# Performance work log

Hardware: AMD Instinct MI355X
Metric: run time of the kernel (lower is better)

The kernel has to match this reference:

```python
import jax, jax.numpy as jnp
import numpy as np

B, N, F = 4, 3000, 128

def setup_inputs() -> dict:
    key = jax.random.key(0)
    k1, k2, k3, k4 = jax.random.split(key, 4)
    x = jax.random.normal(k1, (B, N, F), dtype=jnp.float32)
    adj = jax.random.uniform(k2, (B, N, N), dtype=jnp.float32)
    h0 = jax.random.normal(k3, (B, N, F), dtype=jnp.float32)
    stdv = 1.0 / np.sqrt(F)
    theta = jax.random.uniform(k4, (F, F), dtype=jnp.float32, minval=-stdv, maxval=stdv)
    return {
        "x": x, "adj": adj, "h0": h0, "theta": theta,
        "lamda": jnp.float32(0.5), "alpha": jnp.float32(0.1), "l": 4,
    }

def _normalize_adj(adj):
    # add self loops, then D^{-1/2} A D^{-1/2} via elementwise row/col scaling
    # (same math as diag-embed + inverse + two bmms in the original)
    n = adj.shape[1]
    adj = adj + jnp.eye(n, dtype=adj.dtype)
    deg = jnp.sum(adj, axis=2)                      # [B, N]
    d_inv_sqrt = jax.lax.rsqrt(deg)                 # [B, N]
    return d_inv_sqrt[:, :, None] * adj * d_inv_sqrt[:, None, :]

def reference(x, adj, h0, theta, lamda, alpha, l):
    adj_n = _normalize_adj(adj)
    beta = jnp.log(lamda / l + 1.0)
    hi = jnp.einsum('bnm,bmf->bnf', adj_n, x)       # aggregation
    support = (1.0 - alpha) * hi + alpha * h0       # variant=False path
    r = support
    out = beta * jnp.einsum('bnf,fg->bng', support, theta) + (1.0 - beta) * r
    return out
```

## Files before the change

kernel.cpp:

```cpp
#include <hip/hip_runtime.h>
#include <hip/hip_bf16.h>
#include <math.h>

#define BB 4
#define NN 3000
#define FF 128
#define NKC 96
#define NIT 188

typedef __bf16 bf16x8 __attribute__((ext_vector_type(8)));
typedef float  f32x4  __attribute__((ext_vector_type(4)));

__global__ __launch_bounds__(256) void k_deg(const float* __restrict__ adj,
                                             float* __restrict__ dis) {
    int wid  = (blockIdx.x * 256 + threadIdx.x) >> 6;
    int lane = threadIdx.x & 63;
    if (wid >= BB * NN) return;
    const float4* row = (const float4*)(adj + (size_t)wid * NN);
    float s = 0.f;
    for (int c = lane; c < NN / 4; c += 64) {
        float4 v = row[c];
        s += (v.x + v.y) + (v.z + v.w);
    }
    for (int off = 32; off > 0; off >>= 1) s += __shfl_down(s, off, 64);
    if (lane == 0) dis[wid] = 1.0f / sqrtf(s + 1.0f);
}

__global__ __launch_bounds__(256) void k_xpk(const float* __restrict__ x,
                                             const float* __restrict__ dis,
                                             __bf16* __restrict__ xpk) {
    int b  = blockIdx.y, kc = blockIdx.x;
    int t  = threadIdx.x, w = t >> 6, l = t & 63;
    int m  = l & 15, q = l >> 4;
    #pragma unroll
    for (int h = 0; h < 2; ++h) {
        int nt = w + h * 4;
        int f  = nt * 16 + m;
        bf16x8 v;
        #pragma unroll
        for (int j = 0; j < 8; ++j) {
            int k = kc * 32 + q * 8 + j;
            float val = 0.f;
            if (k < NN) val = dis[b * NN + k] * x[((size_t)b * NN + k) * FF + f];
            v[j] = (__bf16)val;
        }
        *(bf16x8*)(xpk + ((size_t)(b * 8 + nt) * NKC + kc) * 512 + l * 8) = v;
    }
}

__global__ __launch_bounds__(256) void k_thpk(const float* __restrict__ theta,
                                              __bf16* __restrict__ thpk) {
    int kc = blockIdx.x;
    int t  = threadIdx.x, w = t >> 6, l = t & 63;
    int m  = l & 15, q = l >> 4;
    #pragma unroll
    for (int h = 0; h < 2; ++h) {
        int nt = w + h * 4;
        bf16x8 v;
        #pragma unroll
        for (int j = 0; j < 8; ++j) {
            int k = kc * 32 + q * 8 + j;
            v[j] = (__bf16)theta[k * FF + nt * 16 + m];
        }
        *(bf16x8*)(thpk + ((size_t)(nt * 4 + kc)) * 512 + l * 8) = v;
    }
}

__global__ __launch_bounds__(256) void k_agg(const float* __restrict__ adj,
                                             const __bf16* __restrict__ xpk,
                                             const __bf16* __restrict__ thpk,
                                             const float* __restrict__ x,
                                             const float* __restrict__ h0,
                                             const float* __restrict__ dis,
                                             float* __restrict__ out,
                                             const float* __restrict__ alpha_p,
                                             const float* __restrict__ lamda_p,
                                             const int* __restrict__ l_p) {
    __shared__ __bf16 tile[2][16][520];
    __shared__ __bf16 stile[16][136];
    const int b  = blockIdx.y;
    const int it = blockIdx.x;
    const int i0 = it * 16;
    const int t  = threadIdx.x, w = t >> 6, l = t & 63;
    const int m  = l & 15, quad = l >> 4;
    const int n0 = w * 32;
    const __bf16* B0 = xpk + ((size_t)(b * 8 + 2 * w) * NKC) * 512 + l * 8;
    const __bf16* B1 = B0 + (size_t)NKC * 512;
    f32x4 acc0 = {0.f, 0.f, 0.f, 0.f};
    f32x4 acc1 = {0.f, 0.f, 0.f, 0.f};

    float4 pu[4], pv[4];
    auto load_chunk = [&](int c) {
        int k0 = c * 512;
        #pragma unroll
        for (int i = 0; i < 4; ++i) {
            int row  = i * 4 + w;
            int irow = i0 + row;
            int col  = k0 + l * 8;
            float4 u = {0.f, 0.f, 0.f, 0.f}, v = {0.f, 0.f, 0.f, 0.f};
            if (irow < NN && col < NN) {
                const float* p = adj + ((size_t)b * NN + irow) * NN + col;
                u = *(const float4*)p;
                v = *(const float4*)(p + 4);
            }
            pu[i] = u; pv[i] = v;
        }
    };
    auto store_chunk = [&](int cb) {
        #pragma unroll
        for (int i = 0; i < 4; ++i) {
            int row = i * 4 + w;
            bf16x8 s;
            s[0] = (__bf16)pu[i].x; s[1] = (__bf16)pu[i].y;
            s[2] = (__bf16)pu[i].z; s[3] = (__bf16)pu[i].w;
            s[4] = (__bf16)pv[i].x; s[5] = (__bf16)pv[i].y;
            s[6] = (__bf16)pv[i].z; s[7] = (__bf16)pv[i].w;
            *(bf16x8*)&tile[cb][row][l * 8] = s;
        }
    };

    load_chunk(0);
    store_chunk(0);
    __syncthreads();
    for (int c = 0; c < 6; ++c) {
        int cb = c & 1;
        if (c < 5) load_chunk(c + 1);
        #pragma unroll 4
        for (int kcl = 0; kcl < 16; ++kcl) {
            int kc = c * 16 + kcl;
            bf16x8 a  = *(const bf16x8*)&tile[cb][m][kcl * 32 + quad * 8];
            bf16x8 b0 = *(const bf16x8*)(B0 + (size_t)kc * 512);
            bf16x8 b1 = *(const bf16x8*)(B1 + (size_t)kc * 512);
            acc0 = __builtin_amdgcn_mfma_f32_16x16x32_bf16(a, b0, acc0, 0, 0, 0);
            acc1 = __builtin_amdgcn_mfma_f32_16x16x32_bf16(a, b1, acc1, 0, 0, 0);
        }
        if (c < 5) store_chunk(cb ^ 1);
        __syncthreads();
    }

    const float alpha = *alpha_p;
    const float beta  = logf(*lamda_p / (float)(*l_p) + 1.0f);
    float s0v[4], s1v[4];
    #pragma unroll
    for (int r = 0; r < 4; ++r) {
        int row  = quad * 4 + r;
        int irow = i0 + row;
        float s0 = 0.f, s1 = 0.f;
        if (irow < NN) {
            float  di   = dis[b * NN + irow];
            size_t base = ((size_t)b * NN + irow) * FF;
            int c0 = n0 + m, c1 = n0 + 16 + m;
            s0 = (1.f - alpha) * (di * acc0[r] + di * di * x[base + c0]) + alpha * h0[base + c0];
            s1 = (1.f - alpha) * (di * acc1[r] + di * di * x[base + c1]) + alpha * h0[base + c1];
        }
        s0v[r] = s0; s1v[r] = s1;
        stile[row][n0 + m]      = (__bf16)s0;
        stile[row][n0 + 16 + m] = (__bf16)s1;
    }
    __syncthreads();
    f32x4 o0 = {0.f, 0.f, 0.f, 0.f};
    f32x4 o1 = {0.f, 0.f, 0.f, 0.f};
    const __bf16* T0 = thpk + (size_t)(2 * w * 4) * 512 + l * 8;
    const __bf16* T1 = T0 + 4 * 512;
    #pragma unroll
    for (int kc = 0; kc < 4; ++kc) {
        bf16x8 a   = *(const bf16x8*)&stile[m][kc * 32 + quad * 8];
        bf16x8 tb0 = *(const bf16x8*)(T0 + (size_t)kc * 512);
        bf16x8 tb1 = *(const bf16x8*)(T1 + (size_t)kc * 512);
        o0 = __builtin_amdgcn_mfma_f32_16x16x32_bf16(a, tb0, o0, 0, 0, 0);
        o1 = __builtin_amdgcn_mfma_f32_16x16x32_bf16(a, tb1, o1, 0, 0, 0);
    }
    const float omb = 1.f - beta;
    #pragma unroll
    for (int r = 0; r < 4; ++r) {
        int irow = i0 + quad * 4 + r;
        if (irow < NN) {
            size_t base = ((size_t)b * NN + irow) * FF;
            out[base + n0 + m]      = beta * o0[r] + omb * s0v[r];
            out[base + n0 + 16 + m] = beta * o1[r] + omb * s1v[r];
        }
    }
}

extern "C" void kernel_launch(void* const* d_in, const int* in_sizes, int n_in,
                              void* d_out, int out_size, void* d_ws, size_t ws_size,
                              hipStream_t stream) {
    const float* x      = (const float*)d_in[0];
    const float* adj    = (const float*)d_in[1];
    const float* h0     = (const float*)d_in[2];
    const float* theta  = (const float*)d_in[3];
    const float* lamda  = (const float*)d_in[4];
    const float* alpha  = (const float*)d_in[5];
    const int*   l      = (const int*)d_in[6];
    float* out = (float*)d_out;

    char*   ws   = (char*)d_ws;
    float*  dis  = (float*)ws;
    __bf16* xpk  = (__bf16*)(ws + 65536);
    __bf16* thpk = (__bf16*)(ws + 3276800);

    k_deg<<<dim3((BB * NN) / 4), 256, 0, stream>>>(adj, dis);
    k_thpk<<<dim3(4), 256, 0, stream>>>(theta, thpk);
    k_xpk<<<dim3(NKC, BB), 256, 0, stream>>>(x, dis, xpk);
    k_agg<<<dim3(NIT, BB), 256, 0, stream>>>(adj, xpk, thpk, x, h0, dis, out,
                                             alpha, lamda, l);
}
```

Measured before the change: 277.1 us.

## Pre-convert adjacency to padded bf16 in degree pass and async-load into LDS

The degree kernel now also writes a zero-padded bf16 copy of the adjacency matrix (rows padded to 3008, columns to 3072) while it sums each row. The aggregation kernel then reads this bf16 copy and moves it straight into shared memory with global_load_lds, dropping the register round-trip, the fp32-to-bf16 conversion and the bounds checks from its inner pipeline. The aim is to halve the bytes the main kernel reads and to overlap loads with MFMA work more cheaply. In exchange the degree pass writes an extra ~74 MB buffer, the total memory traffic stays about the same, and the code relies on a large workspace.

```diff
diff --git a/kernel.cpp b/kernel.cpp
--- a/kernel.cpp
+++ b/kernel.cpp
@@ -5,25 +5,37 @@
 #define BB 4
 #define NN 3000
 #define FF 128
+#define NP 3008
+#define CP 3072
 #define NKC 96
 #define NIT 188
 
 typedef __bf16 bf16x8 __attribute__((ext_vector_type(8)));
+typedef __bf16 bf16x4 __attribute__((ext_vector_type(4)));
 typedef float  f32x4  __attribute__((ext_vector_type(4)));
 
 __global__ __launch_bounds__(256) void k_deg(const float* __restrict__ adj,
+                                             __bf16* __restrict__ adjh,
                                              float* __restrict__ dis) {
     int wid  = (blockIdx.x * 256 + threadIdx.x) >> 6;
     int lane = threadIdx.x & 63;
-    if (wid >= BB * NN) return;
-    const float4* row = (const float4*)(adj + (size_t)wid * NN);
+    int b = wid / NP, i = wid % NP;
+    bool rowok = i < NN;
+    const float* row = adj + ((size_t)b * NN + (rowok ? i : 0)) * NN;
+    __bf16* drow = adjh + (size_t)wid * CP;
     float s = 0.f;
-    for (int c = lane; c < NN / 4; c += 64) {
-        float4 v = row[c];
+    for (int c = lane; c < CP / 4; c += 64) {
+        int col = c * 4;
+        float4 v = {0.f, 0.f, 0.f, 0.f};
+        if (rowok && col < NN) v = *(const float4*)(row + col);
         s += (v.x + v.y) + (v.z + v.w);
+        bf16x4 h;
+        h[0] = (__bf16)v.x; h[1] = (__bf16)v.y;
+        h[2] = (__bf16)v.z; h[3] = (__bf16)v.w;
+        *(bf16x4*)(drow + col) = h;
     }
     for (int off = 32; off > 0; off >>= 1) s += __shfl_down(s, off, 64);
-    if (lane == 0) dis[wid] = 1.0f / sqrtf(s + 1.0f);
+    if (lane == 0 && rowok) dis[b * NN + i] = 1.0f / sqrtf(s + 1.0f);
 }
 
 __global__ __launch_bounds__(256) void k_xpk(const float* __restrict__ x,
@@ -66,7 +78,7 @@
     }
 }
 
-__global__ __launch_bounds__(256) void k_agg(const float* __restrict__ adj,
+__global__ __launch_bounds__(256) void k_agg(const __bf16* __restrict__ adjh,
                                              const __bf16* __restrict__ xpk,
                                              const __bf16* __restrict__ thpk,
                                              const float* __restrict__ x,
@@ -89,42 +101,23 @@
     f32x4 acc0 = {0.f, 0.f, 0.f, 0.f};
     f32x4 acc1 = {0.f, 0.f, 0.f, 0.f};
 
-    float4 pu[4], pv[4];
-    auto load_chunk = [&](int c) {
-        int k0 = c * 512;
-        #pragma unroll
-        for (int i = 0; i < 4; ++i) {
-            int row  = i * 4 + w;
-            int irow = i0 + row;
-            int col  = k0 + l * 8;
-            float4 u = {0.f, 0.f, 0.f, 0.f}, v = {0.f, 0.f, 0.f, 0.f};
-            if (irow < NN && col < NN) {
-                const float* p = adj + ((size_t)b * NN + irow) * NN + col;
-                u = *(const float4*)p;
-                v = *(const float4*)(p + 4);
-            }
-            pu[i] = u; pv[i] = v;
-        }
-    };
-    auto store_chunk = [&](int cb) {
+    auto issue = [&](int c, int cb) {
         #pragma unroll
         for (int i = 0; i < 4; ++i) {
             int row = i * 4 + w;
-            bf16x8 s;
-            s[0] = (__bf16)pu[i].x; s[1] = (__bf16)pu[i].y;
-            s[2] = (__bf16)pu[i].z; s[3] = (__bf16)pu[i].w;
-            s[4] = (__bf16)pv[i].x; s[5] = (__bf16)pv[i].y;
-            s[6] = (__bf16)pv[i].z; s[7] = (__bf16)pv[i].w;
-            *(bf16x8*)&tile[cb][row][l * 8] = s;
+            const __bf16* g = adjh + ((size_t)(b * NP) + i0 + row) * CP + c * 512 + l * 8;
+            __builtin_amdgcn_global_load_lds(
+                (const __attribute__((address_space(1))) unsigned int*)g,
+                (__attribute__((address_space(3))) unsigned int*)&tile[cb][row][0],
+                16, 0, 0);
         }
     };
 
-    load_chunk(0);
-    store_chunk(0);
+    issue(0, 0);
     __syncthreads();
     for (int c = 0; c < 6; ++c) {
         int cb = c & 1;
-        if (c < 5) load_chunk(c + 1);
+        if (c < 5) issue(c + 1, cb ^ 1);
         #pragma unroll 4
         for (int kcl = 0; kcl < 16; ++kcl) {
             int kc = c * 16 + kcl;
@@ -134,7 +127,6 @@
             acc0 = __builtin_amdgcn_mfma_f32_16x16x32_bf16(a, b0, acc0, 0, 0, 0);
             acc1 = __builtin_amdgcn_mfma_f32_16x16x32_bf16(a, b1, acc1, 0, 0, 0);
         }
-        if (c < 5) store_chunk(cb ^ 1);
         __syncthreads();
     }
 
@@ -198,10 +190,11 @@
     float*  dis  = (float*)ws;
     __bf16* xpk  = (__bf16*)(ws + 65536);
     __bf16* thpk = (__bf16*)(ws + 3276800);
-
-    k_deg<<<dim3((BB * NN) / 4), 256, 0, stream>>>(adj, dis);
+    __bf16* adjh = (__bf16*)(ws + 4 * 1024 * 1024);
+
+    k_deg<<<dim3(BB * NP / 4), 256, 0, stream>>>(adj, adjh, dis);
     k_thpk<<<dim3(4), 256, 0, stream>>>(theta, thpk);
     k_xpk<<<dim3(NKC, BB), 256, 0, stream>>>(x, dis, xpk);
-    k_agg<<<dim3(NIT, BB), 256, 0, stream>>>(adj, xpk, thpk, x, h0, dis, out,
+    k_agg<<<dim3(NIT, BB), 256, 0, stream>>>(adjh, xpk, thpk, x, h0, dis, out,
                                              alpha, lamda, l);
 }
```

Result: slower. 288.9 us (+4.2%).
